# Performance work log

Hardware: AMD Instinct MI355X
Metric: run time of the kernel (lower is better)

The kernel has to match this reference:

```python
import jax, jax.numpy as jnp
import numpy as np
from jax import lax

MAX_ID = 32        # instance ids in the 3d grid are 0..MAX_ID-1
NUM_CLASSES = 13   # semantic labels 0..12 (wall=10, floor=11)
RADIUS = 3
GRID = (256, 256, 256)
SURFACE_THRESH = 1.5
WALL_CLASS, WALL_ID = 10, 1
FLOOR_CLASS, FLOOR_ID = 11, 2
THINGS_START = 2

# offsets in the same lexicographic order as nn_search's triple loop: range(-R, R)
_r = np.arange(-RADIUS, RADIUS)
OFFSETS = np.stack(np.meshgrid(_r, _r, _r, indexing='ij'), -1).reshape(-1, 3).astype(np.int32)


def setup_inputs() -> dict:
    key = jax.random.key(0)
    k1, k2, k3, k4 = jax.random.split(key, 4)
    geometry = jax.random.normal(k1, GRID, dtype=jnp.float32)            # TSDF-like grid
    instances = jax.random.randint(k2, GRID, 0, MAX_ID, dtype=jnp.int32)
    semantics = jax.random.randint(k3, GRID, 0, NUM_CLASSES, dtype=jnp.int32)
    ids2d = jax.random.randint(k4, (16,), 0, MAX_ID, dtype=jnp.int32)    # instances2d['locations'][0]
    return {'geometry': geometry, 'instances': instances, 'semantics': semantics, 'ids2d': ids2d}


def _postprocess(geometry, instances, semantics, ids2d):
    inst_flat = instances.ravel()
    ids2d_p1 = ids2d + 1

    # filter_instances: keep only 3d ids present in (2d instance ids + 1)
    sel_mask = jnp.isin(instances, ids2d_p1)                 # filtered = instances * sel_mask
    zero_present = jnp.any(~sel_mask).astype(jnp.int32)      # does unique(filtered) contain 0?

    # per-id presence; panoptic id = (index of id in unique(filtered)) + THINGS_START
    hist = jnp.bincount(inst_flat, length=MAX_ID + 1)        # voxel count per id
    in2d = jnp.isin(jnp.arange(1, MAX_ID + 1), ids2d_p1)
    present = in2d & (hist[1:] > 0)                          # for ids 1..MAX_ID
    rank = jnp.cumsum(present.astype(jnp.int32))             # 1-based rank among present ids
    pano_ids = jnp.where(present, rank - 1 + zero_present + THINGS_START, 0)
    pano_lut = jnp.zeros(MAX_ID + 1, jnp.int32).at[1:].set(pano_ids)
    panoptic = pano_lut[instances]                           # assign per instances==id masks

    # majority semantic label per instance, excluding {0, wall, floor}
    counts = jnp.zeros((MAX_ID + 1, NUM_CLASSES), jnp.int32).at[inst_flat, semantics.ravel()].add(1)
    counts = counts.at[:, jnp.array([0, WALL_CLASS, FLOOR_CLASS])].set(-1)
    sel_label = jnp.argmax(counts[1:], axis=1).astype(jnp.int32)

    # stuff overrides
    panoptic = jnp.where(semantics == WALL_CLASS, WALL_ID, panoptic)
    panoptic = jnp.where(semantics == FLOOR_CLASS, FLOOR_ID, panoptic)

    surface = jnp.abs(geometry) <= SURFACE_THRESH
    unassigned = surface & (panoptic == 0)
    grid0 = panoptic                                          # panoptic_instances_copy

    def body(carry, off):
        label, found = carry
        shifted = jnp.roll(grid0, shift=-off, axis=(0, 1, 2))  # shifted[p] = grid0[p + off]
        new = (shifted > 0) & ~found
        return (jnp.where(new, shifted, label), found | new), None

    init = (jnp.zeros(GRID, jnp.int32), jnp.zeros(GRID, dtype=bool))
    (nn_label, _), _ = lax.scan(body, init, jnp.asarray(OFFSETS))
    panoptic = jnp.where(unassigned, nn_label, grid0)

    # panoptic id -> semantic label LUT (disjoint ids, order-independent)
    sem_lut = (jnp.zeros(MAX_ID + THINGS_START + 1, jnp.int32)
               .at[WALL_ID].set(WALL_CLASS).at[FLOOR_ID].set(FLOOR_CLASS))
    sem_lut = sem_lut.at[pano_ids].set(jnp.where(present, sel_label, 0))
    panoptic_semantics = sem_lut[panoptic]
    return panoptic, panoptic_semantics


def reference(geometry, instances, semantics, ids2d):
    return jax.jit(_postprocess)(geometry, instances, semantics, ids2d)
```

## Files before the change

### kernel.cpp

```cpp
#include <hip/hip_runtime.h>
#include <stdint.h>

#define GRID_N (256*256*256)
#define MAXID 32
#define NCLS 13
#define NBINS ((MAXID+1)*NCLS)


__global__ __launch_bounds__(256) void k_prep(const float* __restrict__ geo,
                                              const int* __restrict__ inst,
                                              const int* __restrict__ sem,
                                              int* __restrict__ counts,
                                              uint8_t* __restrict__ key) {
    __shared__ int sh[2][NBINS];
    for (int i = threadIdx.x; i < 2 * NBINS; i += blockDim.x) sh[0][i] = 0;
    __syncthreads();
    int* myh = sh[(threadIdx.x >> 6) & 1];
    int tid = blockIdx.x * blockDim.x + threadIdx.x;
    int stride = gridDim.x * blockDim.x;
    const int n4 = GRID_N / 4;
    for (int i = tid; i < n4; i += stride) {
        int4 a = ((const int4*)inst)[i];
        int4 b = ((const int4*)sem)[i];
        float4 g = ((const float4*)geo)[i];
        atomicAdd(&myh[a.x * NCLS + b.x], 1);
        atomicAdd(&myh[a.y * NCLS + b.y], 1);
        atomicAdd(&myh[a.z * NCLS + b.z], 1);
        atomicAdd(&myh[a.w * NCLS + b.w], 1);
        uchar4 k;
        k.x = ((b.x == 11) ? 33 : ((b.x == 10) ? 32 : (uint8_t)a.x)) | (fabsf(g.x) <= 1.5f ? 64 : 0);
        k.y = ((b.y == 11) ? 33 : ((b.y == 10) ? 32 : (uint8_t)a.y)) | (fabsf(g.y) <= 1.5f ? 64 : 0);
        k.z = ((b.z == 11) ? 33 : ((b.z == 10) ? 32 : (uint8_t)a.z)) | (fabsf(g.z) <= 1.5f ? 64 : 0);
        k.w = ((b.w == 11) ? 33 : ((b.w == 10) ? 32 : (uint8_t)a.w)) | (fabsf(g.w) <= 1.5f ? 64 : 0);
        ((uchar4*)key)[i] = k;
    }
    __syncthreads();
    for (int i = threadIdx.x; i < NBINS; i += blockDim.x) {
        int v = sh[0][i] + sh[1][i];
        if (v) atomicAdd(&counts[i], v);
    }
}

__global__ __launch_bounds__(512) void k_luts(const int* __restrict__ counts,
                                              const int* __restrict__ ids2d, int n2d,
                                              int* __restrict__ glut) {
    __shared__ int shc[NBINS];
    __shared__ int hist[MAXID + 1];
    __shared__ int in2d[MAXID + 1];
    __shared__ int sel[MAXID + 1];
    int t = threadIdx.x;
    if (t < NBINS) shc[t] = counts[t];
    __syncthreads();
    if (t <= MAXID) {
        int s = 0;
        for (int c = 0; c < NCLS; ++c) s += shc[t * NCLS + c];
        hist[t] = s;
        int f = 0;
        for (int k = 0; k < n2d; ++k) if (ids2d[k] + 1 == t) f = 1;
        in2d[t] = f;
        int best = -2, bc = 0;
        for (int c = 0; c < NCLS; ++c) {
            int v = (c == 0 || c == 10 || c == 11) ? -1 : shc[t * NCLS + c];
            if (v > best) { best = v; bc = c; }
        }
        sel[t] = bc;
    }
    __syncthreads();
    if (t == 0) {
        int zero_present = 0;
        for (int i = 0; i <= MAXID; ++i)
            if (hist[i] > 0 && !in2d[i]) zero_present = 1;
        int pano_ids[MAXID + 1];
        int present[MAXID + 1];
        glut[0] = 0;
        int rank = 0;
        for (int j = 1; j <= MAXID; ++j) {
            int p = in2d[j] && (hist[j] > 0);
            present[j] = p;
            if (p) rank++;
            pano_ids[j] = p ? (rank - 1 + zero_present + 2) : 0;
            if (j < 32) glut[j] = pano_ids[j];
        }
        glut[32] = 1;
        glut[33] = 2;
        int* sem_lut = glut + 34;
        for (int i = 0; i < MAXID + 3; ++i) sem_lut[i] = 0;
        sem_lut[1] = 10;
        sem_lut[2] = 11;
        for (int j = 1; j <= MAXID; ++j)
            sem_lut[pano_ids[j]] = present[j] ? sel[j] : 0;
    }
}

#define TX 8
#define TY 8
#define HR 13
#define NROWS (HR*HR)
#define ROWDW 66
#define NDW (NROWS*ROWDW)

__global__ __launch_bounds__(512) void k_nn(const uint8_t* __restrict__ key,
                                            const int* __restrict__ glut,
                                            int* __restrict__ out_pano,
                                            int* __restrict__ out_sem) {
    __shared__ uint32_t shg[NDW];
    __shared__ int lut[128];
    __shared__ int slut[MAXID + 3];

    int t = threadIdx.x;
    if (t < 128) {
        int base = ((t & 63) <= 33) ? glut[t & 63] : 0;
        lut[t] = base | ((t & 64) << 1);
    } else if (t >= 128 && t < 128 + MAXID + 3) {
        slut[t - 128] = glut[34 + (t - 128)];
    }
    __syncthreads();

    int x0 = blockIdx.x * TX;
    int y0 = blockIdx.y * TY;

    const uint32_t* key32 = (const uint32_t*)key;
    for (int idx = t; idx < NDW; idx += 512) {
        int row = idx / ROWDW;
        int k = idx - row * ROWDW;
        int ix = row / HR;
        int iy = row - ix * HR;
        int gx = (x0 + ix - 3) & 255;
        int gy = (y0 + iy - 3) & 255;
        uint32_t w = key32[(gx << 14) | (gy << 6) | ((k - 1) & 63)];
        shg[idx] = (uint32_t)lut[w & 127]
                 | ((uint32_t)lut[(w >> 8) & 127] << 8)
                 | ((uint32_t)lut[(w >> 16) & 127] << 16)
                 | ((uint32_t)lut[(w >> 24) & 127] << 24);
    }
    __syncthreads();

    int zg = t & 63;
    int ty = t >> 6;
    int gy = y0 + ty;
    const uint64_t M6 = 0x00007F7F7F7F7F7FULL;

    for (int x = 0; x < TX; ++x) {
        int gx = x0 + x;
        int r0 = (x + 3) * HR + (ty + 3);
        uint32_t cw = shg[r0 * ROWDW + zg + 1];
        int4 pano, semv;
        int pv[4];
        #pragma unroll
        for (int b = 0; b < 4; ++b) {
            int v = (cw >> (8 * b)) & 255;
            int p = v & 127;
            if (p == 0 && (v & 128)) {
                int z = 4 * zg + b;
                int label = 0;
                int j0 = z + 1;
                int a0 = j0 >> 2, off = j0 & 3;
                for (int dxi = 0; dxi < 6 && !label; ++dxi) {
                    int rb = ((x + dxi) * HR + ty) * ROWDW + a0;
                    for (int dyi = 0; dyi < 6; ++dyi) {
                        int a = rb + dyi * ROWDW;
                        uint32_t d0 = shg[a], d1 = shg[a + 1], d2 = shg[a + 2];
                        uint64_t lo = (uint64_t)d0 | ((uint64_t)d1 << 32);
                        uint64_t win = lo >> (off * 8);
                        if (off) win |= (uint64_t)d2 << (64 - off * 8);
                        uint64_t mask = win & M6;
                        if (mask) {
                            int bb = __ffsll((long long)mask) - 1;
                            label = (int)((win >> (bb & 56)) & 0x7f);
                            break;
                        }
                    }
                }
                p = label;
            }
            pv[b] = p;
        }
        pano.x = pv[0]; pano.y = pv[1]; pano.z = pv[2]; pano.w = pv[3];
        semv.x = slut[pv[0]]; semv.y = slut[pv[1]]; semv.z = slut[pv[2]]; semv.w = slut[pv[3]];
        int oi = (gx << 14) | (gy << 6) | zg;
        ((int4*)out_pano)[oi] = pano;
        ((int4*)out_sem)[oi] = semv;
    }
}

extern "C" void kernel_launch(void* const* d_in, const int* in_sizes, int n_in,
                              void* d_out, int out_size, void* d_ws, size_t ws_size,
                              hipStream_t stream) {
    const float* geo   = (const float*)d_in[0];
    const int*   inst  = (const int*)d_in[1];
    const int*   sem   = (const int*)d_in[2];
    const int*   ids2d = (const int*)d_in[3];
    const int    n2d   = in_sizes[3];

    char* ws = (char*)d_ws;
    int* counts  = (int*)(ws);
    int* glut    = (int*)(ws + 4096);
    uint8_t* key = (uint8_t*)(ws + 16384);

    int* out_pano = (int*)d_out;
    int* out_sem  = out_pano + GRID_N;

    hipMemsetAsync(counts, 0, 4096, stream);
    k_prep<<<1024, 256, 0, stream>>>(geo, inst, sem, counts, key);
    k_luts<<<1, 512, 0, stream>>>(counts, ids2d, n2d, glut);
    dim3 g(32, 32);
    k_nn<<<g, 512, 0, stream>>>(key, glut, out_pano, out_sem);
}
```

Before: 309.0 us.

## Widen prep grid, batch loads, spread histogram atomics, parallelize LUT build

The prep kernel now launches 4096 blocks, each thread issuing all four strided vector loads up front before doing the histogram and key work. Each block keeps four per-wavefront shared histograms, and the global counts are split across eight copies to reduce atomic contention. The LUT kernel sums the eight copies and replaces the single-thread serial rank loop with wavefront ballots and popcount. The fixed grid size hardcodes coverage of the whole volume, and more blocks raise the number of final global atomics.

```diff
diff --git a/kernel.cpp b/kernel.cpp
--- a/kernel.cpp
+++ b/kernel.cpp
@@ -5,90 +5,99 @@
 #define MAXID 32
 #define NCLS 13
 #define NBINS ((MAXID+1)*NCLS)
-
-
-__global__ __launch_bounds__(256) void k_prep(const float* __restrict__ geo,
-                                              const int* __restrict__ inst,
-                                              const int* __restrict__ sem,
-                                              int* __restrict__ counts,
-                                              uint8_t* __restrict__ key) {
-    __shared__ int sh[2][NBINS];
-    for (int i = threadIdx.x; i < 2 * NBINS; i += blockDim.x) sh[0][i] = 0;
-    __syncthreads();
-    int* myh = sh[(threadIdx.x >> 6) & 1];
-    int tid = blockIdx.x * blockDim.x + threadIdx.x;
-    int stride = gridDim.x * blockDim.x;
-    const int n4 = GRID_N / 4;
-    for (int i = tid; i < n4; i += stride) {
-        int4 a = ((const int4*)inst)[i];
-        int4 b = ((const int4*)sem)[i];
-        float4 g = ((const float4*)geo)[i];
-        atomicAdd(&myh[a.x * NCLS + b.x], 1);
-        atomicAdd(&myh[a.y * NCLS + b.y], 1);
-        atomicAdd(&myh[a.z * NCLS + b.z], 1);
-        atomicAdd(&myh[a.w * NCLS + b.w], 1);
-        uchar4 k;
-        k.x = ((b.x == 11) ? 33 : ((b.x == 10) ? 32 : (uint8_t)a.x)) | (fabsf(g.x) <= 1.5f ? 64 : 0);
-        k.y = ((b.y == 11) ? 33 : ((b.y == 10) ? 32 : (uint8_t)a.y)) | (fabsf(g.y) <= 1.5f ? 64 : 0);
-        k.z = ((b.z == 11) ? 33 : ((b.z == 10) ? 32 : (uint8_t)a.z)) | (fabsf(g.z) <= 1.5f ? 64 : 0);
-        k.w = ((b.w == 11) ? 33 : ((b.w == 10) ? 32 : (uint8_t)a.w)) | (fabsf(g.w) <= 1.5f ? 64 : 0);
-        ((uchar4*)key)[i] = k;
-    }
-    __syncthreads();
-    for (int i = threadIdx.x; i < NBINS; i += blockDim.x) {
-        int v = sh[0][i] + sh[1][i];
-        if (v) atomicAdd(&counts[i], v);
-    }
-}
-
-__global__ __launch_bounds__(512) void k_luts(const int* __restrict__ counts,
+#define PREP_BLOCKS 4096
+
+
+__device__ __forceinline__ uint8_t keyb(int a, int b, float g) {
+    int k = (b == 11) ? 33 : ((b == 10) ? 32 : a);
+    return (uint8_t)(k | ((fabsf(g) <= 1.5f) ? 64 : 0));
+}
+
+__global__ __launch_bounds__(256, 4) void k_prep(const float* __restrict__ geo,
+                                                 const int* __restrict__ inst,
+                                                 const int* __restrict__ sem,
+                                                 int* __restrict__ counts8,
+                                                 uint8_t* __restrict__ key) {
+    __shared__ int sh[4][NBINS];
+    int t = threadIdx.x;
+    for (int i = t; i < 4 * NBINS; i += 256) ((int*)sh)[i] = 0;
+    __syncthreads();
+    int* myh = sh[t >> 6];
+
+    const int stride = PREP_BLOCKS * 256;
+    int base = blockIdx.x * 256 + t;
+    const int4*  i4 = (const int4*)inst;
+    const int4*  s4 = (const int4*)sem;
+    const float4* g4 = (const float4*)geo;
+
+    int4 a0 = i4[base],            a1 = i4[base + stride],
+         a2 = i4[base + 2*stride], a3 = i4[base + 3*stride];
+    int4 b0 = s4[base],            b1 = s4[base + stride],
+         b2 = s4[base + 2*stride], b3 = s4[base + 3*stride];
+    float4 g0 = g4[base],            g1 = g4[base + stride],
+           g2 = g4[base + 2*stride], g3 = g4[base + 3*stride];
+
+    uchar4* k4 = (uchar4*)key;
+    #define DOIT(A,B,G,IDX)                                                  \
+        atomicAdd(&myh[(A).x * NCLS + (B).x], 1);                            \
+        atomicAdd(&myh[(A).y * NCLS + (B).y], 1);                            \
+        atomicAdd(&myh[(A).z * NCLS + (B).z], 1);                            \
+        atomicAdd(&myh[(A).w * NCLS + (B).w], 1);                            \
+        { uchar4 kk; kk.x = keyb((A).x,(B).x,(G).x);                         \
+          kk.y = keyb((A).y,(B).y,(G).y); kk.z = keyb((A).z,(B).z,(G).z);    \
+          kk.w = keyb((A).w,(B).w,(G).w); k4[IDX] = kk; }
+    DOIT(a0,b0,g0,base)
+    DOIT(a1,b1,g1,base + stride)
+    DOIT(a2,b2,g2,base + 2*stride)
+    DOIT(a3,b3,g3,base + 3*stride)
+    #undef DOIT
+
+    __syncthreads();
+    int* dst = counts8 + (blockIdx.x & 7) * NBINS;
+    for (int i = t; i < NBINS; i += 256) {
+        int v = sh[0][i] + sh[1][i] + sh[2][i] + sh[3][i];
+        if (v) atomicAdd(&dst[i], v);
+    }
+}
+
+__global__ __launch_bounds__(512) void k_luts(const int* __restrict__ counts8,
                                               const int* __restrict__ ids2d, int n2d,
                                               int* __restrict__ glut) {
     __shared__ int shc[NBINS];
-    __shared__ int hist[MAXID + 1];
-    __shared__ int in2d[MAXID + 1];
-    __shared__ int sel[MAXID + 1];
+    __shared__ int sem_s[35];
     int t = threadIdx.x;
-    if (t < NBINS) shc[t] = counts[t];
-    __syncthreads();
-    if (t <= MAXID) {
+    if (t < NBINS) {
         int s = 0;
-        for (int c = 0; c < NCLS; ++c) s += shc[t * NCLS + c];
-        hist[t] = s;
-        int f = 0;
-        for (int k = 0; k < n2d; ++k) if (ids2d[k] + 1 == t) f = 1;
-        in2d[t] = f;
-        int best = -2, bc = 0;
-        for (int c = 0; c < NCLS; ++c) {
-            int v = (c == 0 || c == 10 || c == 11) ? -1 : shc[t * NCLS + c];
-            if (v > best) { best = v; bc = c; }
+        #pragma unroll
+        for (int c = 0; c < 8; ++c) s += counts8[c * NBINS + t];
+        shc[t] = s;
+    }
+    __syncthreads();
+    if (t < 64) {
+        int hist_t = 0, in2d_t = 0, sel_t = 0;
+        if (t <= MAXID) {
+            for (int c = 0; c < NCLS; ++c) hist_t += shc[t * NCLS + c];
+            for (int k = 0; k < n2d; ++k) if (ids2d[k] + 1 == t) in2d_t = 1;
+            int best = -2;
+            for (int c = 0; c < NCLS; ++c) {
+                int v = (c == 0 || c == 10 || c == 11) ? -1 : shc[t * NCLS + c];
+                if (v > best) { best = v; sel_t = c; }
+            }
         }
-        sel[t] = bc;
-    }
-    __syncthreads();
-    if (t == 0) {
-        int zero_present = 0;
-        for (int i = 0; i <= MAXID; ++i)
-            if (hist[i] > 0 && !in2d[i]) zero_present = 1;
-        int pano_ids[MAXID + 1];
-        int present[MAXID + 1];
-        glut[0] = 0;
-        int rank = 0;
-        for (int j = 1; j <= MAXID; ++j) {
-            int p = in2d[j] && (hist[j] > 0);
-            present[j] = p;
-            if (p) rank++;
-            pano_ids[j] = p ? (rank - 1 + zero_present + 2) : 0;
-            if (j < 32) glut[j] = pano_ids[j];
-        }
-        glut[32] = 1;
-        glut[33] = 2;
-        int* sem_lut = glut + 34;
-        for (int i = 0; i < MAXID + 3; ++i) sem_lut[i] = 0;
-        sem_lut[1] = 10;
-        sem_lut[2] = 11;
-        for (int j = 1; j <= MAXID; ++j)
-            sem_lut[pano_ids[j]] = present[j] ? sel[j] : 0;
+        unsigned long long zm = __ballot(t <= MAXID && hist_t > 0 && !in2d_t);
+        int zero_present = (zm != 0ULL) ? 1 : 0;
+        int pres = (t >= 1 && t <= MAXID && in2d_t && hist_t > 0) ? 1 : 0;
+        unsigned long long pm = __ballot(pres);
+        int rank_below = __popcll(pm & ((1ULL << t) - 1ULL));
+        int pano_id = pres ? (rank_below + zero_present + 2) : 0;
+
+        if (t < 35) sem_s[t] = (t == 1) ? 10 : ((t == 2) ? 11 : 0);
+        if (pres) sem_s[pano_id] = sel_t;
+
+        if (t < 32) glut[t] = (t == 0) ? 0 : pano_id;
+        if (t == 32) glut[32] = 1;
+        if (t == 33) glut[33] = 2;
+        if (t < 35) glut[34 + t] = sem_s[t];
     }
 }
 
@@ -193,16 +202,16 @@
     const int    n2d   = in_sizes[3];
 
     char* ws = (char*)d_ws;
-    int* counts  = (int*)(ws);
-    int* glut    = (int*)(ws + 4096);
-    uint8_t* key = (uint8_t*)(ws + 16384);
+    int* counts8 = (int*)(ws);
+    int* glut    = (int*)(ws + 16384);
+    uint8_t* key = (uint8_t*)(ws + 32768);
 
     int* out_pano = (int*)d_out;
     int* out_sem  = out_pano + GRID_N;
 
-    hipMemsetAsync(counts, 0, 4096, stream);
-    k_prep<<<1024, 256, 0, stream>>>(geo, inst, sem, counts, key);
-    k_luts<<<1, 512, 0, stream>>>(counts, ids2d, n2d, glut);
+    hipMemsetAsync(counts8, 0, 16384, stream);
+    k_prep<<<PREP_BLOCKS, 256, 0, stream>>>(geo, inst, sem, counts8, key);
+    k_luts<<<1, 512, 0, stream>>>(counts8, ids2d, n2d, glut);
     dim3 g(32, 32);
     k_nn<<<g, 512, 0, stream>>>(key, glut, out_pano, out_sem);
 }
```

Measured after the change: 305.9 us. About the same (-1.0%).
